# Optimization experiments

Hardware: AMD Instinct MI355X
Metric: run time of the kernel (lower is better)

The kernel has to match this reference:

```python
import jax, jax.numpy as jnp
import numpy as np

B, L, H = 2, 2048, 1536
I, N, R, K = 3072, 16, 96, 4


def setup_inputs() -> dict:
    key = jax.random.key(0)
    ks = jax.random.split(key, 10)
    rn = lambda k, shape, s: jax.random.normal(k, shape, jnp.float32) * s
    return {
        "hidden_states": rn(ks[0], (B, L, H), 1.0),
        "W_in": rn(ks[1], (2 * I, H), 0.02),
        "conv_w": rn(ks[2], (I, K), 0.1),
        "conv_b": rn(ks[3], (I,), 0.1),
        "W_x": rn(ks[4], (R + 2 * N, I), 0.02),
        "W_dt": rn(ks[5], (I, R), 0.02),
        "dt_bias": rn(ks[6], (I,), 0.1),
        # vLLM's weight loader stores A = -exp(A_log); replicate that here
        "A": -jnp.exp(rn(ks[7], (I, N), 0.5)),
        "D": jnp.ones((I,), jnp.float32),
        "W_out": rn(ks[8], (H, I), 0.02),
    }


def reference(hidden_states, W_in, conv_w, conv_b, W_x, W_dt, dt_bias, A, D, W_out):
    b, l, _ = hidden_states.shape
    k = conv_w.shape[1]
    n = A.shape[1]
    r = W_dt.shape[1]

    # in_proj -> [B,L,2I], split into ssm input x and gate
    proj = jnp.einsum("blh,eh->ble", hidden_states, W_in)
    x, gate = jnp.split(proj, 2, axis=-1)  # each [B,L,I]

    # causal depthwise conv1d over L (pad K-1 on the left) + SiLU
    xp = jnp.pad(x, ((0, 0), (k - 1, 0), (0, 0)))
    conv = sum(xp[:, j : j + l, :] * conv_w[:, j] for j in range(k)) + conv_b
    x = jax.nn.silu(conv)  # [B,L,I]

    # x_proj -> dt (rank R), B, C (each N)
    ssm_p = jnp.einsum("bli,pi->blp", x, W_x)
    dt_in, Bm, Cm = jnp.split(ssm_p, [r, r + n], axis=-1)

    # dt_proj (skip_bias_add) then softplus(dt + bias) inside the scan math
    dt = jnp.einsum("blr,ir->bli", dt_in, W_dt)
    delta = jax.nn.softplus(dt + dt_bias)  # [B,L,I]

    # selective scan: s_t = exp(delta_t * A) * s_{t-1} + delta_t * x_t * B_t
    def step(state, inp):
        d_t, u_t, B_t, C_t = inp  # [B,I], [B,I], [B,N], [B,N]
        dA = jnp.exp(d_t[..., None] * A)  # [B,I,N]
        state = state * dA + (d_t * u_t)[..., None] * B_t[:, None, :]
        y = jnp.einsum("bin,bn->bi", state, C_t)
        return state, y

    init = jnp.zeros((b, x.shape[-1], n), jnp.float32)
    _, ys = jax.lax.scan(
        step,
        init,
        (
            delta.transpose(1, 0, 2),
            x.transpose(1, 0, 2),
            Bm.transpose(1, 0, 2),
            Cm.transpose(1, 0, 2),
        ),
    )
    y = ys.transpose(1, 0, 2) + x * D  # skip connection via D
    y = y * jax.nn.silu(gate)

    # out_proj -> [B,L,H]
    return jnp.einsum("bli,hi->blh", y, W_out)
```

## Files before the change

kernel.cpp:

```cpp
#include <hip/hip_runtime.h>

typedef __attribute__((ext_vector_type(8))) short bf16x8;
typedef __attribute__((ext_vector_type(4))) float f32x4;

#define CCH 32
#define TCH 64

__device__ __forceinline__ unsigned short f2b(float f) {
    unsigned u = __float_as_uint(f);
    return (unsigned short)((u + 0x7fffu + ((u >> 16) & 1u)) >> 16);
}
__device__ __forceinline__ float b2f(unsigned short h) {
    return __uint_as_float(((unsigned)h) << 16);
}
__device__ __forceinline__ float softplus_f(float z) {
    return (z > 15.f) ? z : __logf(1.f + __expf(z));
}
__device__ __forceinline__ float silu_f(float g) {
    return g / (1.f + __expf(-g));
}

__device__ __forceinline__ void gload16(const unsigned short* g, unsigned short* l) {
    __builtin_amdgcn_global_load_lds(
        (const __attribute__((address_space(1))) void*)g,
        (__attribute__((address_space(3))) void*)l, 16, 0, 0);
}

__global__ __launch_bounds__(256)
void cast_all(const float* __restrict__ h, const float* __restrict__ win,
              const float* __restrict__ wx, const float* __restrict__ wdt,
              const float* __restrict__ wout,
              unsigned short* __restrict__ dh, unsigned short* __restrict__ dwin,
              unsigned short* __restrict__ dwx, unsigned short* __restrict__ dwdt,
              unsigned short* __restrict__ dwout) {
    const int n0 = 1572864, n1 = n0 + 2359296, n2 = n1 + 98304,
              n3 = n2 + 73728, n4 = n3 + 1179648;
    int i = blockIdx.x * 256 + threadIdx.x;
    const float* s; unsigned short* d; int off;
    if (i < n0)      { s = h;    d = dh;    off = i; }
    else if (i < n1) { s = win;  d = dwin;  off = i - n0; }
    else if (i < n2) { s = wx;   d = dwx;   off = i - n1; }
    else if (i < n3) { s = wdt;  d = dwdt;  off = i - n2; }
    else if (i < n4) { s = wout; d = dwout; off = i - n3; }
    else return;
    float4 v = reinterpret_cast<const float4*>(s)[off];
    ushort4 o;
    o.x = f2b(v.x); o.y = f2b(v.y); o.z = f2b(v.z); o.w = f2b(v.w);
    reinterpret_cast<ushort4*>(d)[off] = o;
}

template <int OP>
__global__ __launch_bounds__(512)
void gemm256(const unsigned short* __restrict__ A, const unsigned short* __restrict__ W,
             void* __restrict__ Cout, int Kc, int lda, int ldw, int ldc,
             int ntx, int silu_col0, long long czs) {
    __shared__ __align__(16) unsigned short lds[65536];
    const int tid  = threadIdx.x;
    const int lane = tid & 63;
    const int wave = tid >> 6;
    const int wr   = wave >> 2;
    const int wc   = wave & 3;
    const int lr   = lane & 15;
    const int quad = lane >> 4;
    const int sw   = lr & 7;

    const int nwg = gridDim.x;
    const int wg  = blockIdx.x;
    const int wgs = (wg & 7) * (nwg >> 3) + (wg >> 3);
    const int bm  = (wgs / ntx) * 256;
    const int bn  = (wgs % ntx) * 256;
    const int kz  = blockIdx.z;
    A += (size_t)kz * Kc;
    W += (size_t)kz * Kc;

    const int rsub = wave * 8 + (lane >> 3);
    const int csw  = ((lane & 7) ^ ((lane >> 3) & 7)) * 8;
    const unsigned short* gA = A + (size_t)(bm + rsub) * lda + csw;
    const unsigned short* gB = W + (size_t)(bn + rsub) * ldw + csw;

#define STA(b, h, kt) do { \
        gload16(gA + (size_t)((h) * 128) * lda + (kt) * 64,      &lds[(b) * 16384 + (h) * 8192 + wave * 512]); \
        gload16(gA + (size_t)((h) * 128 + 64) * lda + (kt) * 64, &lds[(b) * 16384 + (h) * 8192 + 4096 + wave * 512]); \
    } while (0)
#define STB(b, h, kt) do { \
        gload16(gB + (size_t)((h) * 128) * ldw + (kt) * 64,      &lds[32768 + (b) * 16384 + (h) * 8192 + wave * 512]); \
        gload16(gB + (size_t)((h) * 128 + 64) * ldw + (kt) * 64, &lds[32768 + (b) * 16384 + (h) * 8192 + 4096 + wave * 512]); \
    } while (0)

#define LDA_F(b, mh, mi, kk) \
    (*reinterpret_cast<const bf16x8*>(&lds[(b) * 16384 + ((mh) * 128 + wr * 64 + (mi) * 16 + lr) * 64 + (((((kk) << 2) | quad)) ^ sw) * 8]))
#define LDB_F(b, nh, ni, kk) \
    (*reinterpret_cast<const bf16x8*>(&lds[32768 + (b) * 16384 + ((nh) * 128 + wc * 32 + (ni) * 16 + lr) * 64 + (((((kk) << 2) | quad)) ^ sw) * 8]))

#define RD_A(b, mh) do { \
        _Pragma("unroll") for (int mi = 0; mi < 4; ++mi) { \
            fa[mi][0] = LDA_F(b, mh, mi, 0); \
            fa[mi][1] = LDA_F(b, mh, mi, 1); } } while (0)
#define RD_B(b, nh, dst) do { \
        _Pragma("unroll") for (int ni = 0; ni < 2; ++ni) { \
            dst[ni][0] = LDB_F(b, nh, ni, 0); \
            dst[ni][1] = LDB_F(b, nh, ni, 1); } } while (0)

#define MFMA_Q(mh, nh, bb) do { \
        _Pragma("unroll") for (int mi = 0; mi < 4; ++mi) \
        _Pragma("unroll") for (int ni = 0; ni < 2; ++ni) { \
            acc[(mh) * 4 + mi][(nh) * 2 + ni] = __builtin_amdgcn_mfma_f32_16x16x32_bf16(fa[mi][0], bb[ni][0], acc[(mh) * 4 + mi][(nh) * 2 + ni], 0, 0, 0); \
            acc[(mh) * 4 + mi][(nh) * 2 + ni] = __builtin_amdgcn_mfma_f32_16x16x32_bf16(fa[mi][1], bb[ni][1], acc[(mh) * 4 + mi][(nh) * 2 + ni], 0, 0, 0); } } while (0)

#define MIDB  asm volatile("s_barrier" ::: "memory")
#define LGKM0 asm volatile("s_waitcnt lgkmcnt(0)" ::: "memory")
#define ENDB  asm volatile("s_barrier" ::: "memory")
#define ENDB_VM4 asm volatile("s_waitcnt vmcnt(4)\n\ts_barrier" ::: "memory")
#define ENDB_VM0 asm volatile("s_waitcnt vmcnt(0)\n\ts_barrier" ::: "memory")
#define PRIO1 __builtin_amdgcn_s_setprio(1)
#define PRIO0 __builtin_amdgcn_s_setprio(0)

    f32x4 acc[8][4];
    const f32x4 zero = {0.f, 0.f, 0.f, 0.f};
#pragma unroll
    for (int m = 0; m < 8; ++m)
#pragma unroll
        for (int n = 0; n < 4; ++n) acc[m][n] = zero;

    bf16x8 fa[4][2], fb0[2][2], fb1[2][2];

    const int nkt = Kc >> 6;
    const int NT2 = nkt >> 1;

    STA(0, 0, 0); STB(0, 0, 0); STA(0, 1, 0); STB(0, 1, 0);
    STA(1, 0, 1); STB(1, 0, 1);
    ENDB_VM4;

#pragma unroll 1
    for (int t = 0; t < NT2 - 1; ++t) {
        const int k1 = 2 * t + 1, k2 = 2 * t + 2, k3 = 2 * t + 3;
        RD_A(0, 0); RD_B(0, 0, fb0); STA(1, 1, k1);
        MIDB; LGKM0; PRIO1; MFMA_Q(0, 0, fb0); PRIO0; ENDB;
        RD_B(0, 1, fb1); STB(1, 1, k1);
        MIDB; LGKM0; PRIO1; MFMA_Q(0, 1, fb1); PRIO0; ENDB;
        RD_A(0, 1); STA(0, 0, k2);
        MIDB; LGKM0; PRIO1; MFMA_Q(1, 0, fb0); PRIO0; ENDB;
        STB(0, 0, k2);
        MIDB; PRIO1; MFMA_Q(1, 1, fb1); PRIO0; ENDB_VM4;
        RD_A(1, 0); RD_B(1, 0, fb0); STA(0, 1, k2);
        MIDB; LGKM0; PRIO1; MFMA_Q(0, 0, fb0); PRIO0; ENDB;
        RD_B(1, 1, fb1); STB(0, 1, k2);
        MIDB; LGKM0; PRIO1; MFMA_Q(0, 1, fb1); PRIO0; ENDB;
        RD_A(1, 1); STA(1, 0, k3);
        MIDB; LGKM0; PRIO1; MFMA_Q(1, 0, fb0); PRIO0; ENDB;
        STB(1, 0, k3);
        MIDB; PRIO1; MFMA_Q(1, 1, fb1); PRIO0; ENDB_VM4;
    }
    {
        const int k1 = nkt - 1;
        RD_A(0, 0); RD_B(0, 0, fb0); STA(1, 1, k1);
        MIDB; LGKM0; PRIO1; MFMA_Q(0, 0, fb0); PRIO0; ENDB;
        RD_B(0, 1, fb1); STB(1, 1, k1);
        MIDB; LGKM0; PRIO1; MFMA_Q(0, 1, fb1); PRIO0; ENDB;
        RD_A(0, 1);
        MIDB; LGKM0; PRIO1; MFMA_Q(1, 0, fb0); PRIO0; ENDB;
        MIDB; PRIO1; MFMA_Q(1, 1, fb1); PRIO0; ENDB_VM0;
        RD_A(1, 0); RD_B(1, 0, fb0);
        MIDB; LGKM0; PRIO1; MFMA_Q(0, 0, fb0); PRIO0; ENDB;
        RD_B(1, 1, fb1);
        MIDB; LGKM0; PRIO1; MFMA_Q(0, 1, fb1); PRIO0; ENDB;
        RD_A(1, 1);
        MIDB; LGKM0; PRIO1; MFMA_Q(1, 0, fb0); PRIO0; ENDB;
        MIDB; PRIO1; MFMA_Q(1, 1, fb1); PRIO0;
    }

#pragma unroll
    for (int m = 0; m < 8; ++m) {
        const int row0 = bm + (m >> 2) * 128 + wr * 64 + (m & 3) * 16 + quad * 4;
#pragma unroll
        for (int n = 0; n < 4; ++n) {
            const int col = bn + (n >> 1) * 128 + wc * 32 + (n & 1) * 16 + lr;
#pragma unroll
            for (int reg = 0; reg < 4; ++reg) {
                float v = acc[m][n][reg];
                if (OP == 0) {
                    float* Cf = (float*)Cout + (size_t)kz * czs;
                    Cf[(size_t)(row0 + reg) * ldc + col] = v;
                } else {
                    if (col >= silu_col0) v = silu_f(v);
                    ((unsigned short*)Cout)[(size_t)(row0 + reg) * ldc + col] = f2b(v);
                }
            }
        }
    }
#undef STA
#undef STB
#undef LDA_F
#undef LDB_F
#undef RD_A
#undef RD_B
#undef MFMA_Q
#undef MIDB
#undef LGKM0
#undef ENDB
#undef ENDB_VM4
#undef ENDB_VM0
#undef PRIO1
#undef PRIO0
}

__global__ __launch_bounds__(512)
void gemm_out(const unsigned short* __restrict__ A, const unsigned short* __restrict__ W,
              float* __restrict__ Cout, int Kc, int lda, int ldw, int ldc) {
    __shared__ __align__(16) unsigned short A0s[8192];
    __shared__ __align__(16) unsigned short B0s[12288];
    __shared__ __align__(16) unsigned short A1s[8192];
    __shared__ __align__(16) unsigned short B1s[12288];
    const int tid  = threadIdx.x;
    const int lane = tid & 63;
    const int wave = tid >> 6;
    const int wr   = wave >> 2;
    const int wc   = wave & 3;
    const int lr   = lane & 15;
    const int quad = lane >> 4;
    const int sw   = lr & 7;

    const int c  = blockIdx.x & 7;
    const int j  = blockIdx.x >> 3;
    const int bm = j * 128;
    const int bn = c * 192;

    const int rsub = wave * 8 + (lane >> 3);
    const int csw  = ((lane & 7) ^ ((lane >> 3) & 7)) * 8;
    const unsigned short* gA = A + (size_t)(bm + rsub) * lda + csw;
    const unsigned short* gB = W + (size_t)(bn + rsub) * ldw + csw;

#define STAGE_A(ARR, kt) do { \
        gload16(gA + (size_t)0  * lda + (kt) * 64, ARR + 0    + wave * 512); \
        gload16(gA + (size_t)64 * lda + (kt) * 64, ARR + 4096 + wave * 512); \
    } while (0)
#define STAGE_B(ARR, kt) do { \
        gload16(gB + (size_t)0   * ldw + (kt) * 64, ARR + 0    + wave * 512); \
        gload16(gB + (size_t)64  * ldw + (kt) * 64, ARR + 4096 + wave * 512); \
        gload16(gB + (size_t)128 * ldw + (kt) * 64, ARR + 8192 + wave * 512); \
    } while (0)

#define LDA_F(ARR, mi, kk) \
    (*reinterpret_cast<const bf16x8*>(&ARR[(wr * 64 + (mi) * 16 + lr) * 64 + (((((kk) << 2) | quad)) ^ sw) * 8]))
#define LDB_F(ARR, ni, kk) \
    (*reinterpret_cast<const bf16x8*>(&ARR[(wc * 48 + (ni) * 16 + lr) * 64 + (((((kk) << 2) | quad)) ^ sw) * 8]))

#define PRIO1 __builtin_amdgcn_s_setprio(1)
#define PRIO0 __builtin_amdgcn_s_setprio(0)
#define VM0B  asm volatile("s_waitcnt vmcnt(0)\n\ts_barrier" ::: "memory")

#define TILE_BODY(AX, BX) do { \
        _Pragma("unroll") for (int ni = 0; ni < 3; ++ni) { \
            fb[ni][0] = LDB_F(BX, ni, 0); fb[ni][1] = LDB_F(BX, ni, 1); } \
        _Pragma("unroll") for (int mi = 0; mi < 4; ++mi) { \
            fa[mi][0] = LDA_F(AX, mi, 0); fa[mi][1] = LDA_F(AX, mi, 1); } \
        PRIO1; \
        _Pragma("unroll") for (int mi = 0; mi < 4; ++mi) \
        _Pragma("unroll") for (int ni = 0; ni < 3; ++ni) { \
            acc[mi][ni] = __builtin_amdgcn_mfma_f32_16x16x32_bf16(fa[mi][0], fb[ni][0], acc[mi][ni], 0, 0, 0); \
            acc[mi][ni] = __builtin_amdgcn_mfma_f32_16x16x32_bf16(fa[mi][1], fb[ni][1], acc[mi][ni], 0, 0, 0); } \
        PRIO0; \
    } while (0)

    f32x4 acc[4][3];
    const f32x4 zero = {0.f, 0.f, 0.f, 0.f};
#pragma unroll
    for (int m = 0; m < 4; ++m)
#pragma unroll
        for (int n = 0; n < 3; ++n) acc[m][n] = zero;

    bf16x8 fa[4][2], fb[3][2];

    const int nkt = Kc >> 6;

    STAGE_A(A0s, 0); STAGE_B(B0s, 0);
    VM0B;

#pragma unroll 1
    for (int t = 0; t < nkt; t += 2) {
        if (t + 1 < nkt) { STAGE_A(A1s, t + 1); STAGE_B(B1s, t + 1); }
        TILE_BODY(A0s, B0s);
        VM0B;
        if (t + 1 < nkt) {
            if (t + 2 < nkt) { STAGE_A(A0s, t + 2); STAGE_B(B0s, t + 2); }
            TILE_BODY(A1s, B1s);
            VM0B;
        }
    }

#pragma unroll
    for (int mi = 0; mi < 4; ++mi) {
        const int row0 = bm + wr * 64 + mi * 16 + quad * 4;
#pragma unroll
        for (int ni = 0; ni < 3; ++ni) {
            const int col = bn + wc * 48 + ni * 16 + lr;
#pragma unroll
            for (int reg = 0; reg < 4; ++reg)
                Cout[(size_t)(row0 + reg) * ldc + col] = acc[mi][ni][reg];
        }
    }
#undef STAGE_A
#undef STAGE_B
#undef LDA_F
#undef LDB_F
#undef PRIO1
#undef PRIO0
#undef VM0B
#undef TILE_BODY
}

template <int OP>
__global__ __launch_bounds__(256)
void gemm_mfma(const unsigned short* __restrict__ A, const unsigned short* __restrict__ W,
               void* __restrict__ Cout, int Kc, int lda, int ldw, int ldc,
               const float* __restrict__ bias, int silu_col0, long long czs) {
    __shared__ unsigned short As[3][4096];
    __shared__ unsigned short Bs[3][4096];
    const int tid = threadIdx.x;
    const int bm = blockIdx.y * 128;
    const int bn = blockIdx.x * 128;
    const int kz = blockIdx.z;
    A += (size_t)kz * Kc;
    W += (size_t)kz * Kc;
    const int lane = tid & 63;
    const int wave = tid >> 6;
    const int r_a = lane >> 2;
    const int k8 = (lane & 3) * 8;

    const unsigned short* gA0 = A + (size_t)(bm + wave * 16 + r_a) * lda + k8;
    const unsigned short* gA1 = A + (size_t)(bm + 64 + wave * 16 + r_a) * lda + k8;
    const unsigned short* gB0 = W + (size_t)(bn + wave * 16 + r_a) * ldw + k8;
    const unsigned short* gB1 = W + (size_t)(bn + 64 + wave * 16 + r_a) * ldw + k8;

    const int wm = (wave & 1) * 64;
    const int wn = (wave >> 1) * 64;
    const int lr = lane & 15;
    const int quad = lane >> 4;

    f32x4 acc[4][4];
    const f32x4 zero = {0.f, 0.f, 0.f, 0.f};
#pragma unroll
    for (int i = 0; i < 4; i++)
#pragma unroll
        for (int j = 0; j < 4; j++) acc[i][j] = zero;

#define STAGE(koff, j) do { \
        gload16(gA0 + (koff), As[j] + wave * 512); \
        gload16(gA1 + (koff), As[j] + (wave + 4) * 512); \
        gload16(gB0 + (koff), Bs[j] + wave * 512); \
        gload16(gB1 + (koff), Bs[j] + (wave + 4) * 512); \
    } while (0)

    const int niter = Kc >> 5;
    STAGE(0, 0);
    if (niter > 1) STAGE(32, 1);

    int ib = 0;
    for (int k = 0; k < niter; k++) {
        if (k + 1 < niter)
            asm volatile("s_waitcnt vmcnt(4)\n\ts_barrier" ::: "memory");
        else
            asm volatile("s_waitcnt vmcnt(0)\n\ts_barrier" ::: "memory");
        if (k + 2 < niter) {
            int is_ = ib + 2; if (is_ >= 3) is_ -= 3;
            STAGE((k + 2) << 5, is_);
        }
        const unsigned short* as = As[ib];
        const unsigned short* bs = Bs[ib];
        bf16x8 fa[4], fb[4];
#pragma unroll
        for (int mi = 0; mi < 4; mi++)
            fa[mi] = *reinterpret_cast<const bf16x8*>(as + (wm + mi * 16 + lr) * 32 + quad * 8);
#pragma unroll
        for (int ni = 0; ni < 4; ni++)
            fb[ni] = *reinterpret_cast<const bf16x8*>(bs + (wn + ni * 16 + lr) * 32 + quad * 8);
#pragma unroll
        for (int mi = 0; mi < 4; mi++)
#pragma unroll
            for (int ni = 0; ni < 4; ni++)
                acc[mi][ni] = __builtin_amdgcn_mfma_f32_16x16x32_bf16(fa[mi], fb[ni], acc[mi][ni], 0, 0, 0);
        ib = (ib == 2) ? 0 : ib + 1;
    }
#undef STAGE

#pragma unroll
    for (int mi = 0; mi < 4; mi++)
#pragma unroll
        for (int reg = 0; reg < 4; reg++) {
            int row = bm + wm + mi * 16 + quad * 4 + reg;
#pragma unroll
            for (int ni = 0; ni < 4; ni++) {
                int col = bn + wn + ni * 16 + lr;
                float v = acc[mi][ni][reg];
                if (OP == 0) {
                    float* Cf = (float*)Cout + (size_t)kz * czs;
                    Cf[(size_t)row * ldc + col] = v;
                } else if (OP == 2) {
                    if (col >= silu_col0) v = silu_f(v);
                    ((unsigned short*)Cout)[(size_t)row * ldc + col] = f2b(v);
                } else {
                    ((unsigned short*)Cout)[(size_t)row * ldc + col] = f2b(softplus_f(v + bias[col]));
                }
            }
        }
}

__global__ __launch_bounds__(256)
void reduce_xpart(const float* __restrict__ xpart, float* __restrict__ ssmp,
                  unsigned short* __restrict__ dtin) {
    const int BL = 4096;
    int idx = blockIdx.x * 256 + threadIdx.x;
    int row = idx >> 5;
    int c4 = (idx & 31) * 4;
    float4 s = {0.f, 0.f, 0.f, 0.f};
#pragma unroll
    for (int z = 0; z < 8; z++) {
        float4 v = *reinterpret_cast<const float4*>(xpart + (size_t)z * BL * 128 + (size_t)row * 128 + c4);
        s.x += v.x; s.y += v.y; s.z += v.z; s.w += v.w;
    }
    *reinterpret_cast<float4*>(ssmp + (size_t)row * 128 + c4) = s;
    if (c4 < 96) {
        ushort4 o;
        o.x = f2b(s.x); o.y = f2b(s.y); o.z = f2b(s.z); o.w = f2b(s.w);
        *reinterpret_cast<ushort4*>(dtin + (size_t)row * 96 + c4) = o;
    }
}

__global__ __launch_bounds__(256)
void conv_silu8(const unsigned short* __restrict__ projbf, const float* __restrict__ cw,
                const float* __restrict__ cb, unsigned short* __restrict__ xc) {
    const int I = 3072, L = 2048, LD = 6144;
    int idx = blockIdx.x * 256 + threadIdx.x;
    int i8 = (idx % (I / 8)) * 8;
    int bl = idx / (I / 8);
    int l = bl & (L - 1);
    float s[8];
    {
        float4 b0 = *reinterpret_cast<const float4*>(cb + i8);
        float4 b1 = *reinterpret_cast<const float4*>(cb + i8 + 4);
        s[0]=b0.x; s[1]=b0.y; s[2]=b0.z; s[3]=b0.w; s[4]=b1.x; s[5]=b1.y; s[6]=b1.z; s[7]=b1.w;
    }
    float w[8][4];
#pragma unroll
    for (int c = 0; c < 8; c++) {
        float4 wr = *reinterpret_cast<const float4*>(cw + (i8 + c) * 4);
        w[c][0]=wr.x; w[c][1]=wr.y; w[c][2]=wr.z; w[c][3]=wr.w;
    }
#pragma unroll
    for (int j = 0; j < 4; j++) {
        if (l + j - 3 >= 0) {
            uint4 r = *reinterpret_cast<const uint4*>(projbf + (size_t)(bl + j - 3) * LD + i8);
            float xv[8];
            xv[0]=b2f((unsigned short)(r.x & 0xffff)); xv[1]=b2f((unsigned short)(r.x >> 16));
            xv[2]=b2f((unsigned short)(r.y & 0xffff)); xv[3]=b2f((unsigned short)(r.y >> 16));
            xv[4]=b2f((unsigned short)(r.z & 0xffff)); xv[5]=b2f((unsigned short)(r.z >> 16));
            xv[6]=b2f((unsigned short)(r.w & 0xffff)); xv[7]=b2f((unsigned short)(r.w >> 16));
#pragma unroll
            for (int c = 0; c < 8; c++) s[c] = fmaf(xv[c], w[c][j], s[c]);
        }
    }
    unsigned short o[8];
#pragma unroll
    for (int c = 0; c < 8; c++) o[c] = f2b(silu_f(s[c]));
    uint4 packed;
    packed.x = (unsigned)o[0] | ((unsigned)o[1] << 16);
    packed.y = (unsigned)o[2] | ((unsigned)o[3] << 16);
    packed.z = (unsigned)o[4] | ((unsigned)o[5] << 16);
    packed.w = (unsigned)o[6] | ((unsigned)o[7] << 16);
    *reinterpret_cast<uint4*>(xc + (size_t)bl * I + i8) = packed;
}

__global__ __launch_bounds__(256)
void scan_passA(const unsigned short* __restrict__ delta_bf, const unsigned short* __restrict__ xc,
                const float* __restrict__ ssmp, const float* __restrict__ Aw,
                float* __restrict__ S_local, float* __restrict__ sumDelta) {
    const int I = 3072, L = 2048;
    __shared__ float bc[TCH][32];
    int g = blockIdx.x * 256 + threadIdx.x;
    int i = g % I;
    int bcid = g / I;
    int c = bcid % CCH;
    int b = bcid / CCH;
    size_t rowbase = (size_t)b * L + (size_t)c * TCH;
    for (int e = threadIdx.x; e < TCH * 8; e += 256) {
        int t = e >> 3, q = e & 7;
        float4 v = *reinterpret_cast<const float4*>(ssmp + (rowbase + t) * 128 + 96 + q * 4);
        *reinterpret_cast<float4*>(&bc[t][q * 4]) = v;
    }
    __syncthreads();

    float Arow[16];
#pragma unroll
    for (int n = 0; n < 16; n++) Arow[n] = Aw[i * 16 + n];
    float st[16];
#pragma unroll
    for (int n = 0; n < 16; n++) st[n] = 0.f;
    float sumD = 0.f;

    size_t rowI = rowbase * I + i;
    for (int t = 0; t < TCH; t++) {
        float delta = b2f(delta_bf[rowI]);
        float du = delta * b2f(xc[rowI]);
        sumD += delta;
        float4 b0 = *reinterpret_cast<const float4*>(&bc[t][0]);
        float4 b1 = *reinterpret_cast<const float4*>(&bc[t][4]);
        float4 b2 = *reinterpret_cast<const float4*>(&bc[t][8]);
        float4 b3 = *reinterpret_cast<const float4*>(&bc[t][12]);
        const float bv[16] = {b0.x,b0.y,b0.z,b0.w, b1.x,b1.y,b1.z,b1.w,
                              b2.x,b2.y,b2.z,b2.w, b3.x,b3.y,b3.z,b3.w};
#pragma unroll
        for (int n = 0; n < 16; n++)
            st[n] = fmaf(st[n], __expf(delta * Arow[n]), du * bv[n]);
        rowI += I;
    }
    size_t obase = (size_t)bcid * 16 * I + i;
#pragma unroll
    for (int n = 0; n < 16; n++) S_local[obase + (size_t)n * I] = st[n];
    sumDelta[(size_t)bcid * I + i] = sumD;
}

__global__ __launch_bounds__(256)
void scan_passB(const float* __restrict__ S_local, const float* __restrict__ sumDelta,
                const float* __restrict__ Aw, float* __restrict__ state_in) {
    const int I = 3072;
    int g = blockIdx.x * 256 + threadIdx.x;
    int i = g % I;
    int bn = g / I;
    int n = bn & 15;
    int b = bn >> 4;
    float a = Aw[i * 16 + n];
    float state = 0.f;
    for (int c = 0; c < CCH; c++) {
        int bcid = b * CCH + c;
        size_t idx = ((size_t)bcid * 16 + n) * I + i;
        state_in[idx] = state;
        state = fmaf(state, __expf(a * sumDelta[(size_t)bcid * I + i]), S_local[idx]);
    }
}

__global__ __launch_bounds__(256)
void scan_passC(const unsigned short* __restrict__ projbf,
                const unsigned short* __restrict__ xc,
                const float* __restrict__ ssmp, const unsigned short* __restrict__ delta_bf,
                const float* __restrict__ Aw, const float* __restrict__ Dw,
                const float* __restrict__ state_in, unsigned short* __restrict__ ybf) {
    const int I = 3072, L = 2048, LD = 6144;
    __shared__ float bc[TCH][32];
    int g = blockIdx.x * 256 + threadIdx.x;
    int i = g % I;
    int bcid = g / I;
    int c = bcid % CCH;
    int b = bcid / CCH;
    size_t rowbase = (size_t)b * L + (size_t)c * TCH;
    for (int e = threadIdx.x; e < TCH * 8; e += 256) {
        int t = e >> 3, q = e & 7;
        float4 v = *reinterpret_cast<const float4*>(ssmp + (rowbase + t) * 128 + 96 + q * 4);
        *reinterpret_cast<float4*>(&bc[t][q * 4]) = v;
    }
    __syncthreads();

    float Arow[16];
#pragma unroll
    for (int n = 0; n < 16; n++) Arow[n] = Aw[i * 16 + n];
    float Dv = Dw[i];
    float st[16];
    size_t sbase = (size_t)bcid * 16 * I + i;
#pragma unroll
    for (int n = 0; n < 16; n++) st[n] = state_in[sbase + (size_t)n * I];

    size_t rowI = rowbase * I + i;
    size_t rowG = rowbase * LD + I + i;
    for (int t = 0; t < TCH; t++) {
        float delta = b2f(delta_bf[rowI]);
        float u = b2f(xc[rowI]);
        float du = delta * u;
        float4 b0 = *reinterpret_cast<const float4*>(&bc[t][0]);
        float4 b1 = *reinterpret_cast<const float4*>(&bc[t][4]);
        float4 b2 = *reinterpret_cast<const float4*>(&bc[t][8]);
        float4 b3 = *reinterpret_cast<const float4*>(&bc[t][12]);
        float4 c0 = *reinterpret_cast<const float4*>(&bc[t][16]);
        float4 c1 = *reinterpret_cast<const float4*>(&bc[t][20]);
        float4 c2 = *reinterpret_cast<const float4*>(&bc[t][24]);
        float4 c3 = *reinterpret_cast<const float4*>(&bc[t][28]);
        const float bv[16] = {b0.x,b0.y,b0.z,b0.w, b1.x,b1.y,b1.z,b1.w,
                              b2.x,b2.y,b2.z,b2.w, b3.x,b3.y,b3.z,b3.w};
        const float cv[16] = {c0.x,c0.y,c0.z,c0.w, c1.x,c1.y,c1.z,c1.w,
                              c2.x,c2.y,c2.z,c2.w, c3.x,c3.y,c3.z,c3.w};
        float y = 0.f;
#pragma unroll
        for (int n = 0; n < 16; n++) {
            st[n] = fmaf(st[n], __expf(delta * Arow[n]), du * bv[n]);
            y = fmaf(st[n], cv[n], y);
        }
        y = fmaf(u, Dv, y);
        y *= b2f(projbf[rowG]);
        ybf[rowI] = f2b(y);
        rowI += I;
        rowG += LD;
    }
}

extern "C" void kernel_launch(void* const* d_in, const int* in_sizes, int n_in,
                              void* d_out, int out_size, void* d_ws, size_t ws_size,
                              hipStream_t stream) {
    const float* hidden  = (const float*)d_in[0];
    const float* W_in    = (const float*)d_in[1];
    const float* conv_w  = (const float*)d_in[2];
    const float* conv_b  = (const float*)d_in[3];
    const float* W_x     = (const float*)d_in[4];
    const float* W_dt    = (const float*)d_in[5];
    const float* dt_bias = (const float*)d_in[6];
    const float* Aw      = (const float*)d_in[7];
    const float* Dw      = (const float*)d_in[8];
    const float* W_out   = (const float*)d_in[9];
    float* out = (float*)d_out;

    constexpr int Bsz = 2, L = 2048, H = 1536, I = 3072, R = 96;
    constexpr int BL = Bsz * L;
    constexpr int TwoI = 2 * I;

    char* base = (char*)d_ws;
    unsigned short* proj_bf  = (unsigned short*)base; base += (size_t)BL * TwoI * 2;
    unsigned short* delta_bf = (unsigned short*)base; base += (size_t)BL * I * 2;
    unsigned short* xc_bf    = (unsigned short*)base; base += (size_t)BL * I * 2;
    unsigned short* y_bf     = (unsigned short*)base; base += (size_t)BL * I * 2;
    float* ssmp              = (float*)base;          base += (size_t)BL * 128 * 4;
    float* xpart             = (float*)base;          base += (size_t)8 * BL * 128 * 4;
    unsigned short* dtin_bf  = (unsigned short*)base; base += (size_t)BL * R * 2;
    unsigned short* wx_bf    = (unsigned short*)base; base += (size_t)128 * I * 2;
    unsigned short* wdt_bf   = (unsigned short*)base; base += (size_t)I * R * 2;
    unsigned short* wout_bf  = (unsigned short*)base; base += (size_t)H * I * 2;
    unsigned short* h_bf     = (unsigned short*)base; base += (size_t)BL * H * 2;
    unsigned short* win_bf   = (unsigned short*)base; base += (size_t)TwoI * H * 2;
    float* S_local  = (float*)h_bf;
    float* sumDelta = S_local + (size_t)Bsz * CCH * 16 * I;
    float* state_in = sumDelta + (size_t)Bsz * CCH * I;

    dim3 blk(256);

    cast_all<<<(5283840 + 255) / 256, blk, 0, stream>>>(
        hidden, W_in, W_x, W_dt, W_out, h_bf, win_bf, wx_bf, wdt_bf, wout_bf);

    gemm256<2><<<dim3(24 * 16, 1, 1), dim3(512), 0, stream>>>(
        h_bf, win_bf, proj_bf, H, H, H, TwoI,  TwoI / 256,  I, 0);

    conv_silu8<<<BL * I / 8 / 256, blk, 0, stream>>>(proj_bf, conv_w, conv_b, xc_bf);

    gemm_mfma<0><<<dim3(1, BL / 128, 8), blk, 0, stream>>>(
        xc_bf, wx_bf, xpart, I / 8, I, I, 128, nullptr, 0, (long long)BL * 128);
    reduce_xpart<<<BL * 32 / 256, blk, 0, stream>>>(xpart, ssmp, dtin_bf);

    gemm_mfma<3><<<dim3(I / 128, BL / 128, 1), blk, 0, stream>>>(
        dtin_bf, wdt_bf, delta_bf, R, R, R, I, dt_bias, 0, 0);

    scan_passA<<<Bsz * I * CCH / 256, blk, 0, stream>>>(
        delta_bf, xc_bf, ssmp, Aw, S_local, sumDelta);
    scan_passB<<<Bsz * 16 * I / 256, blk, 0, stream>>>(
        S_local, sumDelta, Aw, state_in);
    scan_passC<<<Bsz * I * CCH / 256, blk, 0, stream>>>(
        proj_bf, xc_bf, ssmp, delta_bf, Aw, Dw, state_in, y_bf);

    gemm_out<<<dim3(256, 1, 1), dim3(512), 0, stream>>>(
        y_bf, wout_bf, out, I, I, I, H);
}
```

Baseline: 461.8 us.

## Retile in-projection GEMM to 256x384 tiles and process two channels per scan thread

Replaces the 256x256 in-proj GEMM with a 256x384, K=32 double-buffered kernel launched as exactly 256 workgroups, with simpler waits and two blocks per CU. Separately, scan passes A and C now have each thread handle two channels (i and i+HI), halving the grid and reusing the B/C LDS reads and loop overhead across both channels. The GEMM change aims to fill the CUs in a single wave and cut barrier overhead. The cost is more registers per thread (48 accumulators in the GEMM, 64 state floats in the scan), which can lower occupancy. Shallower K steps also mean more barriers per unit of work.

```diff
diff --git a/kernel.cpp b/kernel.cpp
--- a/kernel.cpp
+++ b/kernel.cpp
@@ -49,12 +49,14 @@
     reinterpret_cast<ushort4*>(d)[off] = o;
 }
 
-template <int OP>
-__global__ __launch_bounds__(512)
-void gemm256(const unsigned short* __restrict__ A, const unsigned short* __restrict__ W,
-             void* __restrict__ Cout, int Kc, int lda, int ldw, int ldc,
-             int ntx, int silu_col0, long long czs) {
-    __shared__ __align__(16) unsigned short lds[65536];
+__global__ __launch_bounds__(512, 2)
+void gemm_in(const unsigned short* __restrict__ A, const unsigned short* __restrict__ W,
+             unsigned short* __restrict__ Cout, int Kc, int lda, int ldw, int ldc,
+             int silu_col0) {
+    __shared__ __align__(16) unsigned short A0s[8192];
+    __shared__ __align__(16) unsigned short B0s[12288];
+    __shared__ __align__(16) unsigned short A1s[8192];
+    __shared__ __align__(16) unsigned short B1s[12288];
     const int tid  = threadIdx.x;
     const int lane = tid & 63;
     const int wave = tid >> 6;
@@ -62,146 +64,97 @@
     const int wc   = wave & 3;
     const int lr   = lane & 15;
     const int quad = lane >> 4;
-    const int sw   = lr & 7;
-
-    const int nwg = gridDim.x;
-    const int wg  = blockIdx.x;
-    const int wgs = (wg & 7) * (nwg >> 3) + (wg >> 3);
-    const int bm  = (wgs / ntx) * 256;
-    const int bn  = (wgs % ntx) * 256;
-    const int kz  = blockIdx.z;
-    A += (size_t)kz * Kc;
-    W += (size_t)kz * Kc;
-
-    const int rsub = wave * 8 + (lane >> 3);
-    const int csw  = ((lane & 7) ^ ((lane >> 3) & 7)) * 8;
+    const int sw2  = lr & 3;
+
+    const int c  = blockIdx.x & 7;
+    const int j  = blockIdx.x >> 3;
+    const int bn = (c * 2 + (j & 1)) * 384;
+    const int bm = (j >> 1) * 256;
+
+    const int rsub = wave * 16 + (lane >> 2);
+    const int csw  = ((lane & 3) ^ ((lane >> 2) & 3)) * 8;
     const unsigned short* gA = A + (size_t)(bm + rsub) * lda + csw;
     const unsigned short* gB = W + (size_t)(bn + rsub) * ldw + csw;
 
-#define STA(b, h, kt) do { \
-        gload16(gA + (size_t)((h) * 128) * lda + (kt) * 64,      &lds[(b) * 16384 + (h) * 8192 + wave * 512]); \
-        gload16(gA + (size_t)((h) * 128 + 64) * lda + (kt) * 64, &lds[(b) * 16384 + (h) * 8192 + 4096 + wave * 512]); \
+#define STAGE_A(ARR, kt) do { \
+        gload16(gA + (size_t)0   * lda + (kt) * 32, ARR + wave * 512); \
+        gload16(gA + (size_t)128 * lda + (kt) * 32, ARR + 4096 + wave * 512); \
     } while (0)
-#define STB(b, h, kt) do { \
-        gload16(gB + (size_t)((h) * 128) * ldw + (kt) * 64,      &lds[32768 + (b) * 16384 + (h) * 8192 + wave * 512]); \
-        gload16(gB + (size_t)((h) * 128 + 64) * ldw + (kt) * 64, &lds[32768 + (b) * 16384 + (h) * 8192 + 4096 + wave * 512]); \
+#define STAGE_B(ARR, kt) do { \
+        gload16(gB + (size_t)0   * ldw + (kt) * 32, ARR + wave * 512); \
+        gload16(gB + (size_t)128 * ldw + (kt) * 32, ARR + 4096 + wave * 512); \
+        gload16(gB + (size_t)256 * ldw + (kt) * 32, ARR + 8192 + wave * 512); \
     } while (0)
 
-#define LDA_F(b, mh, mi, kk) \
-    (*reinterpret_cast<const bf16x8*>(&lds[(b) * 16384 + ((mh) * 128 + wr * 64 + (mi) * 16 + lr) * 64 + (((((kk) << 2) | quad)) ^ sw) * 8]))
-#define LDB_F(b, nh, ni, kk) \
-    (*reinterpret_cast<const bf16x8*>(&lds[32768 + (b) * 16384 + ((nh) * 128 + wc * 32 + (ni) * 16 + lr) * 64 + (((((kk) << 2) | quad)) ^ sw) * 8]))
-
-#define RD_A(b, mh) do { \
-        _Pragma("unroll") for (int mi = 0; mi < 4; ++mi) { \
-            fa[mi][0] = LDA_F(b, mh, mi, 0); \
-            fa[mi][1] = LDA_F(b, mh, mi, 1); } } while (0)
-#define RD_B(b, nh, dst) do { \
-        _Pragma("unroll") for (int ni = 0; ni < 2; ++ni) { \
-            dst[ni][0] = LDB_F(b, nh, ni, 0); \
-            dst[ni][1] = LDB_F(b, nh, ni, 1); } } while (0)
-
-#define MFMA_Q(mh, nh, bb) do { \
-        _Pragma("unroll") for (int mi = 0; mi < 4; ++mi) \
-        _Pragma("unroll") for (int ni = 0; ni < 2; ++ni) { \
-            acc[(mh) * 4 + mi][(nh) * 2 + ni] = __builtin_amdgcn_mfma_f32_16x16x32_bf16(fa[mi][0], bb[ni][0], acc[(mh) * 4 + mi][(nh) * 2 + ni], 0, 0, 0); \
-            acc[(mh) * 4 + mi][(nh) * 2 + ni] = __builtin_amdgcn_mfma_f32_16x16x32_bf16(fa[mi][1], bb[ni][1], acc[(mh) * 4 + mi][(nh) * 2 + ni], 0, 0, 0); } } while (0)
-
-#define MIDB  asm volatile("s_barrier" ::: "memory")
-#define LGKM0 asm volatile("s_waitcnt lgkmcnt(0)" ::: "memory")
-#define ENDB  asm volatile("s_barrier" ::: "memory")
-#define ENDB_VM4 asm volatile("s_waitcnt vmcnt(4)\n\ts_barrier" ::: "memory")
-#define ENDB_VM0 asm volatile("s_waitcnt vmcnt(0)\n\ts_barrier" ::: "memory")
+#define LDA_F(ARR, mi) \
+    (*reinterpret_cast<const bf16x8*>(&ARR[(wr * 128 + (mi) * 16 + lr) * 32 + ((quad ^ sw2)) * 8]))
+#define LDB_F(ARR, ni) \
+    (*reinterpret_cast<const bf16x8*>(&ARR[(wc * 96 + (ni) * 16 + lr) * 32 + ((quad ^ sw2)) * 8]))
+
 #define PRIO1 __builtin_amdgcn_s_setprio(1)
 #define PRIO0 __builtin_amdgcn_s_setprio(0)
-
-    f32x4 acc[8][4];
+#define VM0B  asm volatile("s_waitcnt vmcnt(0)\n\ts_barrier" ::: "memory")
+
+#define TILE_BODY(AX, BX) do { \
+        _Pragma("unroll") for (int ni = 0; ni < 6; ++ni) fb[ni] = LDB_F(BX, ni); \
+        _Pragma("unroll") for (int mp = 0; mp < 4; ++mp) { \
+            bf16x8 fa0 = LDA_F(AX, 2 * mp); \
+            bf16x8 fa1 = LDA_F(AX, 2 * mp + 1); \
+            PRIO1; \
+            _Pragma("unroll") for (int ni = 0; ni < 6; ++ni) { \
+                acc[2 * mp][ni]     = __builtin_amdgcn_mfma_f32_16x16x32_bf16(fa0, fb[ni], acc[2 * mp][ni], 0, 0, 0); \
+                acc[2 * mp + 1][ni] = __builtin_amdgcn_mfma_f32_16x16x32_bf16(fa1, fb[ni], acc[2 * mp + 1][ni], 0, 0, 0); } \
+            PRIO0; } \
+    } while (0)
+
+    f32x4 acc[8][6];
     const f32x4 zero = {0.f, 0.f, 0.f, 0.f};
 #pragma unroll
     for (int m = 0; m < 8; ++m)
 #pragma unroll
-        for (int n = 0; n < 4; ++n) acc[m][n] = zero;
-
-    bf16x8 fa[4][2], fb0[2][2], fb1[2][2];
-
-    const int nkt = Kc >> 6;
-    const int NT2 = nkt >> 1;
-
-    STA(0, 0, 0); STB(0, 0, 0); STA(0, 1, 0); STB(0, 1, 0);
-    STA(1, 0, 1); STB(1, 0, 1);
-    ENDB_VM4;
+        for (int n = 0; n < 6; ++n) acc[m][n] = zero;
+
+    bf16x8 fb[6];
+
+    const int nkt = Kc >> 5;
+
+    STAGE_A(A0s, 0); STAGE_B(B0s, 0);
+    VM0B;
 
 #pragma unroll 1
-    for (int t = 0; t < NT2 - 1; ++t) {
-        const int k1 = 2 * t + 1, k2 = 2 * t + 2, k3 = 2 * t + 3;
-        RD_A(0, 0); RD_B(0, 0, fb0); STA(1, 1, k1);
-        MIDB; LGKM0; PRIO1; MFMA_Q(0, 0, fb0); PRIO0; ENDB;
-        RD_B(0, 1, fb1); STB(1, 1, k1);
-        MIDB; LGKM0; PRIO1; MFMA_Q(0, 1, fb1); PRIO0; ENDB;
-        RD_A(0, 1); STA(0, 0, k2);
-        MIDB; LGKM0; PRIO1; MFMA_Q(1, 0, fb0); PRIO0; ENDB;
-        STB(0, 0, k2);
-        MIDB; PRIO1; MFMA_Q(1, 1, fb1); PRIO0; ENDB_VM4;
-        RD_A(1, 0); RD_B(1, 0, fb0); STA(0, 1, k2);
-        MIDB; LGKM0; PRIO1; MFMA_Q(0, 0, fb0); PRIO0; ENDB;
-        RD_B(1, 1, fb1); STB(0, 1, k2);
-        MIDB; LGKM0; PRIO1; MFMA_Q(0, 1, fb1); PRIO0; ENDB;
-        RD_A(1, 1); STA(1, 0, k3);
-        MIDB; LGKM0; PRIO1; MFMA_Q(1, 0, fb0); PRIO0; ENDB;
-        STB(1, 0, k3);
-        MIDB; PRIO1; MFMA_Q(1, 1, fb1); PRIO0; ENDB_VM4;
-    }
-    {
-        const int k1 = nkt - 1;
-        RD_A(0, 0); RD_B(0, 0, fb0); STA(1, 1, k1);
-        MIDB; LGKM0; PRIO1; MFMA_Q(0, 0, fb0); PRIO0; ENDB;
-        RD_B(0, 1, fb1); STB(1, 1, k1);
-        MIDB; LGKM0; PRIO1; MFMA_Q(0, 1, fb1); PRIO0; ENDB;
-        RD_A(0, 1);
-        MIDB; LGKM0; PRIO1; MFMA_Q(1, 0, fb0); PRIO0; ENDB;
-        MIDB; PRIO1; MFMA_Q(1, 1, fb1); PRIO0; ENDB_VM0;
-        RD_A(1, 0); RD_B(1, 0, fb0);
-        MIDB; LGKM0; PRIO1; MFMA_Q(0, 0, fb0); PRIO0; ENDB;
-        RD_B(1, 1, fb1);
-        MIDB; LGKM0; PRIO1; MFMA_Q(0, 1, fb1); PRIO0; ENDB;
-        RD_A(1, 1);
-        MIDB; LGKM0; PRIO1; MFMA_Q(1, 0, fb0); PRIO0; ENDB;
-        MIDB; PRIO1; MFMA_Q(1, 1, fb1); PRIO0;
-    }
-
-#pragma unroll
-    for (int m = 0; m < 8; ++m) {
-        const int row0 = bm + (m >> 2) * 128 + wr * 64 + (m & 3) * 16 + quad * 4;
-#pragma unroll
-        for (int n = 0; n < 4; ++n) {
-            const int col = bn + (n >> 1) * 128 + wc * 32 + (n & 1) * 16 + lr;
+    for (int t = 0; t < nkt; t += 2) {
+        if (t + 1 < nkt) { STAGE_A(A1s, t + 1); STAGE_B(B1s, t + 1); }
+        TILE_BODY(A0s, B0s);
+        VM0B;
+        if (t + 1 < nkt) {
+            if (t + 2 < nkt) { STAGE_A(A0s, t + 2); STAGE_B(B0s, t + 2); }
+            TILE_BODY(A1s, B1s);
+            VM0B;
+        }
+    }
+
+#pragma unroll
+    for (int mi = 0; mi < 8; ++mi) {
+        const int row0 = bm + wr * 128 + mi * 16 + quad * 4;
+#pragma unroll
+        for (int ni = 0; ni < 6; ++ni) {
+            const int col = bn + wc * 96 + ni * 16 + lr;
 #pragma unroll
             for (int reg = 0; reg < 4; ++reg) {
-                float v = acc[m][n][reg];
-                if (OP == 0) {
-                    float* Cf = (float*)Cout + (size_t)kz * czs;
-                    Cf[(size_t)(row0 + reg) * ldc + col] = v;
-                } else {
-                    if (col >= silu_col0) v = silu_f(v);
-                    ((unsigned short*)Cout)[(size_t)(row0 + reg) * ldc + col] = f2b(v);
-                }
+                float v = acc[mi][ni][reg];
+                if (col >= silu_col0) v = silu_f(v);
+                Cout[(size_t)(row0 + reg) * ldc + col] = f2b(v);
             }
         }
     }
-#undef STA
-#undef STB
+#undef STAGE_A
+#undef STAGE_B
 #undef LDA_F
 #undef LDB_F
-#undef RD_A
-#undef RD_B
-#undef MFMA_Q
-#undef MIDB
-#undef LGKM0
-#undef ENDB
-#undef ENDB_VM4
-#undef ENDB_VM0
 #undef PRIO1
 #undef PRIO0
+#undef VM0B
+#undef TILE_BODY
 }
 
 __global__ __launch_bounds__(512)
@@ -474,49 +427,59 @@
 void scan_passA(const unsigned short* __restrict__ delta_bf, const unsigned short* __restrict__ xc,
                 const float* __restrict__ ssmp, const float* __restrict__ Aw,
                 float* __restrict__ S_local, float* __restrict__ sumDelta) {
-    const int I = 3072, L = 2048;
-    __shared__ float bc[TCH][32];
+    const int I = 3072, L = 2048, HI = 1536;
+    __shared__ float bc[TCH][16];
     int g = blockIdx.x * 256 + threadIdx.x;
-    int i = g % I;
-    int bcid = g / I;
+    int i = g % HI;
+    int bcid = g / HI;
     int c = bcid % CCH;
     int b = bcid / CCH;
     size_t rowbase = (size_t)b * L + (size_t)c * TCH;
-    for (int e = threadIdx.x; e < TCH * 8; e += 256) {
-        int t = e >> 3, q = e & 7;
+    {
+        int e = threadIdx.x;
+        int t = e >> 2, q = e & 3;
         float4 v = *reinterpret_cast<const float4*>(ssmp + (rowbase + t) * 128 + 96 + q * 4);
         *reinterpret_cast<float4*>(&bc[t][q * 4]) = v;
     }
     __syncthreads();
 
-    float Arow[16];
-#pragma unroll
-    for (int n = 0; n < 16; n++) Arow[n] = Aw[i * 16 + n];
-    float st[16];
-#pragma unroll
-    for (int n = 0; n < 16; n++) st[n] = 0.f;
-    float sumD = 0.f;
+    float A0[16], A1[16], s0[16], s1[16];
+#pragma unroll
+    for (int n = 0; n < 16; n++) {
+        A0[n] = Aw[i * 16 + n];
+        A1[n] = Aw[(i + HI) * 16 + n];
+        s0[n] = 0.f; s1[n] = 0.f;
+    }
+    float sum0 = 0.f, sum1 = 0.f;
 
     size_t rowI = rowbase * I + i;
     for (int t = 0; t < TCH; t++) {
-        float delta = b2f(delta_bf[rowI]);
-        float du = delta * b2f(xc[rowI]);
-        sumD += delta;
+        float d0 = b2f(delta_bf[rowI]);
+        float d1 = b2f(delta_bf[rowI + HI]);
+        float du0 = d0 * b2f(xc[rowI]);
+        float du1 = d1 * b2f(xc[rowI + HI]);
+        sum0 += d0; sum1 += d1;
         float4 b0 = *reinterpret_cast<const float4*>(&bc[t][0]);
-        float4 b1 = *reinterpret_cast<const float4*>(&bc[t][4]);
+        float4 b1v = *reinterpret_cast<const float4*>(&bc[t][4]);
         float4 b2 = *reinterpret_cast<const float4*>(&bc[t][8]);
         float4 b3 = *reinterpret_cast<const float4*>(&bc[t][12]);
-        const float bv[16] = {b0.x,b0.y,b0.z,b0.w, b1.x,b1.y,b1.z,b1.w,
+        const float bv[16] = {b0.x,b0.y,b0.z,b0.w, b1v.x,b1v.y,b1v.z,b1v.w,
                               b2.x,b2.y,b2.z,b2.w, b3.x,b3.y,b3.z,b3.w};
 #pragma unroll
-        for (int n = 0; n < 16; n++)
-            st[n] = fmaf(st[n], __expf(delta * Arow[n]), du * bv[n]);
+        for (int n = 0; n < 16; n++) {
+            s0[n] = fmaf(s0[n], __expf(d0 * A0[n]), du0 * bv[n]);
+            s1[n] = fmaf(s1[n], __expf(d1 * A1[n]), du1 * bv[n]);
+        }
         rowI += I;
     }
     size_t obase = (size_t)bcid * 16 * I + i;
 #pragma unroll
-    for (int n = 0; n < 16; n++) S_local[obase + (size_t)n * I] = st[n];
-    sumDelta[(size_t)bcid * I + i] = sumD;
+    for (int n = 0; n < 16; n++) {
+        S_local[obase + (size_t)n * I]      = s0[n];
+        S_local[obase + (size_t)n * I + HI] = s1[n];
+    }
+    sumDelta[(size_t)bcid * I + i]      = sum0;
+    sumDelta[(size_t)bcid * I + i + HI] = sum1;
 }
 
 __global__ __launch_bounds__(256)
@@ -544,11 +507,11 @@
                 const float* __restrict__ ssmp, const unsigned short* __restrict__ delta_bf,
                 const float* __restrict__ Aw, const float* __restrict__ Dw,
                 const float* __restrict__ state_in, unsigned short* __restrict__ ybf) {
-    const int I = 3072, L = 2048, LD = 6144;
+    const int I = 3072, L = 2048, LD = 6144, HI = 1536;
     __shared__ float bc[TCH][32];
     int g = blockIdx.x * 256 + threadIdx.x;
-    int i = g % I;
-    int bcid = g / I;
+    int i = g % HI;
+    int bcid = g / HI;
     int c = bcid % CCH;
     int b = bcid / CCH;
     size_t rowbase = (size_t)b * L + (size_t)c * TCH;
@@ -559,42 +522,54 @@
     }
     __syncthreads();
 
-    float Arow[16];
-#pragma unroll
-    for (int n = 0; n < 16; n++) Arow[n] = Aw[i * 16 + n];
-    float Dv = Dw[i];
-    float st[16];
+    float A0[16], A1[16], s0[16], s1[16];
+#pragma unroll
+    for (int n = 0; n < 16; n++) {
+        A0[n] = Aw[i * 16 + n];
+        A1[n] = Aw[(i + HI) * 16 + n];
+    }
+    float D0 = Dw[i], D1 = Dw[i + HI];
     size_t sbase = (size_t)bcid * 16 * I + i;
 #pragma unroll
-    for (int n = 0; n < 16; n++) st[n] = state_in[sbase + (size_t)n * I];
+    for (int n = 0; n < 16; n++) {
+        s0[n] = state_in[sbase + (size_t)n * I];
+        s1[n] = state_in[sbase + (size_t)n * I + HI];
+    }
 
     size_t rowI = rowbase * I + i;
     size_t rowG = rowbase * LD + I + i;
     for (int t = 0; t < TCH; t++) {
-        float delta = b2f(delta_bf[rowI]);
-        float u = b2f(xc[rowI]);
-        float du = delta * u;
-        float4 b0 = *reinterpret_cast<const float4*>(&bc[t][0]);
-        float4 b1 = *reinterpret_cast<const float4*>(&bc[t][4]);
-        float4 b2 = *reinterpret_cast<const float4*>(&bc[t][8]);
-        float4 b3 = *reinterpret_cast<const float4*>(&bc[t][12]);
-        float4 c0 = *reinterpret_cast<const float4*>(&bc[t][16]);
-        float4 c1 = *reinterpret_cast<const float4*>(&bc[t][20]);
-        float4 c2 = *reinterpret_cast<const float4*>(&bc[t][24]);
-        float4 c3 = *reinterpret_cast<const float4*>(&bc[t][28]);
-        const float bv[16] = {b0.x,b0.y,b0.z,b0.w, b1.x,b1.y,b1.z,b1.w,
-                              b2.x,b2.y,b2.z,b2.w, b3.x,b3.y,b3.z,b3.w};
-        const float cv[16] = {c0.x,c0.y,c0.z,c0.w, c1.x,c1.y,c1.z,c1.w,
-                              c2.x,c2.y,c2.z,c2.w, c3.x,c3.y,c3.z,c3.w};
-        float y = 0.f;
+        float d0 = b2f(delta_bf[rowI]);
+        float d1 = b2f(delta_bf[rowI + HI]);
+        float u0 = b2f(xc[rowI]);
+        float u1 = b2f(xc[rowI + HI]);
+        float du0 = d0 * u0, du1 = d1 * u1;
+        float4 v0 = *reinterpret_cast<const float4*>(&bc[t][0]);
+        float4 v1 = *reinterpret_cast<const float4*>(&bc[t][4]);
+        float4 v2 = *reinterpret_cast<const float4*>(&bc[t][8]);
+        float4 v3 = *reinterpret_cast<const float4*>(&bc[t][12]);
+        float4 w0 = *reinterpret_cast<const float4*>(&bc[t][16]);
+        float4 w1 = *reinterpret_cast<const float4*>(&bc[t][20]);
+        float4 w2 = *reinterpret_cast<const float4*>(&bc[t][24]);
+        float4 w3 = *reinterpret_cast<const float4*>(&bc[t][28]);
+        const float bv[16] = {v0.x,v0.y,v0.z,v0.w, v1.x,v1.y,v1.z,v1.w,
+                              v2.x,v2.y,v2.z,v2.w, v3.x,v3.y,v3.z,v3.w};
+        const float cv[16] = {w0.x,w0.y,w0.z,w0.w, w1.x,w1.y,w1.z,w1.w,
+                              w2.x,w2.y,w2.z,w2.w, w3.x,w3.y,w3.z,w3.w};
+        float y0 = 0.f, y1 = 0.f;
 #pragma unroll
         for (int n = 0; n < 16; n++) {
-            st[n] = fmaf(st[n], __expf(delta * Arow[n]), du * bv[n]);
-            y = fmaf(st[n], cv[n], y);
-        }
-        y = fmaf(u, Dv, y);
-        y *= b2f(projbf[rowG]);
-        ybf[rowI] = f2b(y);
+            s0[n] = fmaf(s0[n], __expf(d0 * A0[n]), du0 * bv[n]);
+            s1[n] = fmaf(s1[n], __expf(d1 * A1[n]), du1 * bv[n]);
+            y0 = fmaf(s0[n], cv[n], y0);
+            y1 = fmaf(s1[n], cv[n], y1);
+        }
+        y0 = fmaf(u0, D0, y0);
+        y1 = fmaf(u1, D1, y1);
+        y0 *= b2f(projbf[rowG]);
+        y1 *= b2f(projbf[rowG + HI]);
+        ybf[rowI]      = f2b(y0);
+        ybf[rowI + HI] = f2b(y1);
         rowI += I;
         rowG += LD;
     }
@@ -641,8 +616,8 @@
     cast_all<<<(5283840 + 255) / 256, blk, 0, stream>>>(
         hidden, W_in, W_x, W_dt, W_out, h_bf, win_bf, wx_bf, wdt_bf, wout_bf);
 
-    gemm256<2><<<dim3(24 * 16, 1, 1), dim3(512), 0, stream>>>(
-        h_bf, win_bf, proj_bf, H, H, H, TwoI,  TwoI / 256,  I, 0);
+    gemm_in<<<dim3(256, 1, 1), dim3(512), 0, stream>>>(
+        h_bf, win_bf, proj_bf, H, H, H, TwoI,  I);
 
     conv_silu8<<<BL * I / 8 / 256, blk, 0, stream>>>(proj_bf, conv_w, conv_b, xc_bf);
 
@@ -653,11 +628,11 @@
     gemm_mfma<3><<<dim3(I / 128, BL / 128, 1), blk, 0, stream>>>(
         dtin_bf, wdt_bf, delta_bf, R, R, R, I, dt_bias, 0, 0);
 
-    scan_passA<<<Bsz * I * CCH / 256, blk, 0, stream>>>(
+    scan_passA<<<Bsz * CCH * (I / 2) / 256, blk, 0, stream>>>(
         delta_bf, xc_bf, ssmp, Aw, S_local, sumDelta);
     scan_passB<<<Bsz * 16 * I / 256, blk, 0, stream>>>(
         S_local, sumDelta, Aw, state_in);
-    scan_passC<<<Bsz * I * CCH / 256, blk, 0, stream>>>(
+    scan_passC<<<Bsz * CCH * (I / 2) / 256, blk, 0, stream>>>(
         proj_bf, xc_bf, ssmp, delta_bf, Aw, Dw, state_in, y_bf);
 
     gemm_out<<<dim3(256, 1, 1), dim3(512), 0, stream>>>(
```

After: 478.7 us. +3.7%, slower.
